# Kernel tuning notes

Hardware: AMD Instinct MI355X
Metric: run time of the kernel (lower is better)

## Reference

```python
import jax, jax.numpy as jnp
import numpy as np

NUM_TAGS = 64
HIDDEN = 768
INTERMEDIATE = 3072
TAGGING_RATE = 1.0
LN_EPS = 1e-12


def layer_norm(x, g, b):
    mu = jnp.mean(x, axis=-1, keepdims=True)
    var = jnp.mean(jnp.square(x - mu), axis=-1, keepdims=True)
    return (x - mu) * jax.lax.rsqrt(var + LN_EPS) * g + b


def setup_inputs() -> dict:
    key = jax.random.key(0)
    ks = jax.random.split(key, 16)
    B, S, H, I = 8, 4096, HIDDEN, INTERMEDIATE
    s = 0.02
    return {
        "word_embedding": jax.random.normal(ks[0], (B, S, H), jnp.float32),
        "token_tags": jax.random.randint(ks[1], (B, S), 0, NUM_TAGS, jnp.int32),
        "tag_mask": jax.random.randint(ks[2], (B, S), 0, 2, jnp.int32),
        # learned params
        "tag_emb": jax.random.normal(ks[3], (NUM_TAGS, H), jnp.float32) * s,
        "Wv": jax.random.normal(ks[4], (H, H), jnp.float32) * s,   # v_proj (applied as x @ Wv)
        "bv": jnp.zeros((H,), jnp.float32),
        "Wo": jax.random.normal(ks[5], (H, H), jnp.float32) * s,   # out_proj
        "bo": jnp.zeros((H,), jnp.float32),
        "ln1_g": jnp.ones((H,), jnp.float32),
        "ln1_b": jnp.zeros((H,), jnp.float32),
        "W1": jax.random.normal(ks[6], (H, I), jnp.float32) * s,
        "b1": jnp.zeros((I,), jnp.float32),
        "W2": jax.random.normal(ks[7], (I, H), jnp.float32) * s,
        "b2": jnp.zeros((H,), jnp.float32),
        "ln2_g": jnp.ones((H,), jnp.float32),
        "ln2_b": jnp.zeros((H,), jnp.float32),
    }


def reference(word_embedding, token_tags, tag_mask, tag_emb, Wv, bv, Wo, bo,
              ln1_g, ln1_b, W1, b1, W2, b2, ln2_g, ln2_b):
    # MHA with a single key/value: softmax over one key == 1 for every head,
    # so attention_output = out_proj(v_proj(tag_embedding[tag])), independent of q.
    per_tag = (tag_emb @ Wv + bv) @ Wo + bo              # [num_tags, H]
    taged = per_tag[token_tags] * tag_mask[..., None].astype(word_embedding.dtype)  # [B,S,H]
    x = word_embedding + taged * TAGGING_RATE            # dropout is identity in eval
    x = layer_norm(x, ln1_g, ln1_b)
    ff = jax.nn.relu(x @ W1 + b1) @ W2 + b2              # feed_forward
    out = layer_norm(ff + x, ln2_g, ln2_b)
    return out
```

## Files before the change

### kernel.cpp

```cpp
#include <hip/hip_runtime.h>
#include <hip/hip_bf16.h>
#include <cstdint>
#include <cstddef>

typedef __hip_bfloat16 bf16;
typedef __attribute__((ext_vector_type(8))) short short8;
typedef __attribute__((ext_vector_type(4))) float f32x4;

__device__ __forceinline__ void gload_lds16(const void* g, void* l) {
    __builtin_amdgcn_global_load_lds((const __attribute__((address_space(1))) void*)g,
                                     (__attribute__((address_space(3))) void*)l,
                                     16, 0, 0);
}

__device__ __forceinline__ void vm_wait6() { asm volatile("s_waitcnt vmcnt(6)" ::: "memory"); }
__device__ __forceinline__ void vm_wait0() { asm volatile("s_waitcnt vmcnt(0)" ::: "memory"); }
#define SBAR  asm volatile("s_barrier" ::: "memory")
#define LGKM0 asm volatile("s_waitcnt lgkmcnt(0)" ::: "memory")

__device__ __forceinline__ unsigned short f2bf_bits(float f) {
    bf16 h = __float2bfloat16(f);
    return *reinterpret_cast<unsigned short*>(&h);
}

__global__ __launch_bounds__(256)
void transpose_cvt(const float* __restrict__ in, bf16* __restrict__ out, int R, int C)
{
    __shared__ float tile[32][33];
    const int tx = threadIdx.x & 31;
    const int ty = threadIdx.x >> 5;
    const int c0 = blockIdx.x * 32;
    const int r0 = blockIdx.y * 32;
    #pragma unroll
    for (int j = 0; j < 32; j += 8)
        tile[ty + j][tx] = in[(size_t)(r0 + ty + j) * C + c0 + tx];
    __syncthreads();
    #pragma unroll
    for (int j = 0; j < 32; j += 8)
        out[(size_t)(c0 + ty + j) * R + r0 + tx] = __float2bfloat16(tile[tx][ty + j]);
}

__global__ __launch_bounds__(256)
void tag_gemm_a(const float* __restrict__ te, const float* __restrict__ Wv,
                const float* __restrict__ bv, float* __restrict__ t1)
{
    const int idx = blockIdx.x * 256 + threadIdx.x;
    const int i = idx / 768, j = idx - i * 768;
    float acc = bv[j];
    const float* a = te + (size_t)i * 768;
    for (int k = 0; k < 768; ++k)
        acc += a[k] * Wv[(size_t)k * 768 + j];
    t1[idx] = acc;
}

__global__ __launch_bounds__(256)
void tag_gemm_b(const float* __restrict__ t1, const float* __restrict__ Wo,
                const float* __restrict__ bo, float* __restrict__ ptab)
{
    const int idx = blockIdx.x * 256 + threadIdx.x;
    const int i = idx / 768, j = idx - i * 768;
    float acc = bo[j];
    const float* a = t1 + (size_t)i * 768;
    for (int k = 0; k < 768; ++k)
        acc += a[k] * Wo[(size_t)k * 768 + j];
    ptab[idx] = acc;
}

__global__ __launch_bounds__(192)
void addtag_ln(const float* __restrict__ we, const int* __restrict__ tags,
               const int* __restrict__ mask, const float* __restrict__ ptab,
               const float* __restrict__ g, const float* __restrict__ b,
               bf16* __restrict__ out)
{
    const int row = blockIdx.x;
    const int t = threadIdx.x;
    const int lane = t & 63, wid = t >> 6;
    const float msk = (float)mask[row];
    const float4 wv = ((const float4*)(we + (size_t)row * 768))[t];
    const float4 pv = ((const float4*)(ptab + (size_t)tags[row] * 768))[t];
    float4 x;
    x.x = wv.x + msk * pv.x;  x.y = wv.y + msk * pv.y;
    x.z = wv.z + msk * pv.z;  x.w = wv.w + msk * pv.w;
    float s  = x.x + x.y + x.z + x.w;
    float s2 = x.x * x.x + x.y * x.y + x.z * x.z + x.w * x.w;
    #pragma unroll
    for (int o = 32; o > 0; o >>= 1) { s += __shfl_down(s, o); s2 += __shfl_down(s2, o); }
    __shared__ float ls[3], ls2[3];
    if (lane == 0) { ls[wid] = s; ls2[wid] = s2; }
    __syncthreads();
    s  = ls[0] + ls[1] + ls[2];
    s2 = ls2[0] + ls2[1] + ls2[2];
    const float mean = s * (1.f / 768.f);
    float var = s2 * (1.f / 768.f) - mean * mean;
    var = var < 0.f ? 0.f : var;
    const float inv = 1.f / sqrtf(var + 1e-12f);
    const float4 gv = ((const float4*)g)[t];
    const float4 bv = ((const float4*)b)[t];
    uint2 o2;
    o2.x = (unsigned)f2bf_bits((x.x - mean) * inv * gv.x + bv.x)
         | ((unsigned)f2bf_bits((x.y - mean) * inv * gv.y + bv.y) << 16);
    o2.y = (unsigned)f2bf_bits((x.z - mean) * inv * gv.z + bv.z)
         | ((unsigned)f2bf_bits((x.w - mean) * inv * gv.w + bv.w) << 16);
    ((uint2*)(out + (size_t)row * 768))[t] = o2;
}

__global__ __launch_bounds__(192)
void ln_inplace(float* __restrict__ y, const float* __restrict__ g, const float* __restrict__ b)
{
    const int row = blockIdx.x;
    const int t = threadIdx.x;
    const int lane = t & 63, wid = t >> 6;
    float4* yr = (float4*)(y + (size_t)row * 768);
    const float4 x = yr[t];
    float s  = x.x + x.y + x.z + x.w;
    float s2 = x.x * x.x + x.y * x.y + x.z * x.z + x.w * x.w;
    #pragma unroll
    for (int o = 32; o > 0; o >>= 1) { s += __shfl_down(s, o); s2 += __shfl_down(s2, o); }
    __shared__ float ls[3], ls2[3];
    if (lane == 0) { ls[wid] = s; ls2[wid] = s2; }
    __syncthreads();
    s  = ls[0] + ls[1] + ls[2];
    s2 = ls2[0] + ls2[1] + ls2[2];
    const float mean = s * (1.f / 768.f);
    float var = s2 * (1.f / 768.f) - mean * mean;
    var = var < 0.f ? 0.f : var;
    const float inv = 1.f / sqrtf(var + 1e-12f);
    const float4 gv = ((const float4*)g)[t];
    const float4 bv = ((const float4*)b)[t];
    float4 o;
    o.x = (x.x - mean) * inv * gv.x + bv.x;
    o.y = (x.y - mean) * inv * gv.y + bv.y;
    o.z = (x.z - mean) * inv * gv.z + bv.z;
    o.w = (x.w - mean) * inv * gv.w + bv.w;
    yr[t] = o;
}

template<int EPI, typename OutT>
__global__ __launch_bounds__(512, 2)
void gemm256(const bf16* __restrict__ A, const bf16* __restrict__ Bt,
             const float* __restrict__ bias, const bf16* __restrict__ resid,
             OutT* __restrict__ C, int N, int K, int nbx)
{
    extern __shared__ char smem[];
    char* const AsB = smem;
    char* const BsB = smem + 65536;

    const int t    = threadIdx.x;
    const int lane = t & 63;
    const int wid  = t >> 6;
    const int quad = lane >> 4;
    const int lr   = lane & 15;
    const int wmRow = (wid >> 2) * 128;
    const int wnRow = (wid & 3) * 64;

    const int nwg = gridDim.x;
    const int swz = (blockIdx.x & 7) * (nwg >> 3) + (blockIdx.x >> 3);
    const int bx = swz % nbx;
    const int by = swz / nbx;
    const int rowBase = by * 256;
    const int colBase = bx * 256;

    const char* const Ab = (const char*)(A + (size_t)rowBase * K);
    const char* const Bb = (const char*)(Bt + (size_t)colBase * K);
    const int strideB = K * 2;
    const int nkt = K >> 6;

    f32x4 acc[8][4] = {};

    const int i0 = t, i1 = t + 512;
    const int r0 = i0 >> 3, r1 = i1 >> 3;
    const int sc0 = ((i0 & 7) ^ (r0 & 7)) * 16;
    const int sc1 = ((i1 & 7) ^ (r1 & 7)) * 16;

    #define STAGE_A(buf_, kt_, h_) do {                                          \
        const int kb_ = (kt_) * 128;                                             \
        gload_lds16(Ab + (size_t)((h_)*128 + r0) * strideB + kb_ + sc0,          \
                    AsB + (buf_)*32768 + (h_)*16384 + i0*16);                    \
        gload_lds16(Ab + (size_t)((h_)*128 + r1) * strideB + kb_ + sc1,          \
                    AsB + (buf_)*32768 + (h_)*16384 + i1*16);                    \
    } while (0)
    #define STAGE_B(buf_, kt_, h_) do {                                          \
        const int kb_ = (kt_) * 128;                                             \
        gload_lds16(Bb + (size_t)((h_)*128 + r0) * strideB + kb_ + sc0,          \
                    BsB + (buf_)*32768 + (h_)*16384 + i0*16);                    \
        gload_lds16(Bb + (size_t)((h_)*128 + r1) * strideB + kb_ + sc1,          \
                    BsB + (buf_)*32768 + (h_)*16384 + i1*16);                    \
    } while (0)

    short8 af0[8], af1[8], bf0[4], bf1[4];
    #define RD_A(buf_, ks_, dst_) do {                                           \
        const int cch_ = (ks_)*4 + quad;                                         \
        _Pragma("unroll")                                                        \
        for (int mi = 0; mi < 8; ++mi) {                                         \
            const int R_ = wmRow + mi*16 + lr;                                   \
            dst_[mi] = *(const short8*)(AsB + (buf_)*32768 + R_*128 +            \
                                        ((cch_ ^ (R_ & 7)) * 16));               \
        }                                                                        \
    } while (0)
    #define RD_B(buf_, ks_, dst_) do {                                           \
        const int cch_ = (ks_)*4 + quad;                                         \
        _Pragma("unroll")                                                        \
        for (int ni = 0; ni < 4; ++ni) {                                         \
            const int R_ = wnRow + ni*16 + lr;                                   \
            dst_[ni] = *(const short8*)(BsB + (buf_)*32768 + R_*128 +            \
                                        ((cch_ ^ (R_ & 7)) * 16));               \
        }                                                                        \
    } while (0)
    #define MFMA8x2(AF_, BF_, n0_) do {                                          \
        __builtin_amdgcn_s_setprio(1);                                           \
        _Pragma("unroll")                                                        \
        for (int mi = 0; mi < 8; ++mi) {                                         \
            acc[mi][(n0_)]   = __builtin_amdgcn_mfma_f32_16x16x32_bf16(          \
                AF_[mi], BF_[(n0_)],   acc[mi][(n0_)],   0, 0, 0);               \
            acc[mi][(n0_)+1] = __builtin_amdgcn_mfma_f32_16x16x32_bf16(          \
                AF_[mi], BF_[(n0_)+1], acc[mi][(n0_)+1], 0, 0, 0);               \
        }                                                                        \
        __builtin_amdgcn_s_setprio(0);                                           \
    } while (0)

    STAGE_A(0, 0, 0); STAGE_A(0, 0, 1); STAGE_B(0, 0, 0); STAGE_B(0, 0, 1);
    if (nkt > 1) { STAGE_A(1, 1, 0); STAGE_A(1, 1, 1); STAGE_B(1, 1, 0); }

    for (int kt = 0; kt < nkt; ++kt) {
        const int buf = kt & 1;
        if (kt == nkt - 1) vm_wait0(); else vm_wait6();
        SBAR;
        RD_A(buf, 0, af0);
        RD_B(buf, 0, bf0);
        if (kt + 1 < nkt) STAGE_B(buf ^ 1, kt + 1, 1);
        MFMA8x2(af0, bf0, 0);
        SBAR;
        RD_A(buf, 1, af1);
        RD_B(buf, 1, bf1);
        MFMA8x2(af0, bf0, 2);
        LGKM0;
        SBAR;
        if (kt + 2 < nkt) { STAGE_A(buf, kt + 2, 0); STAGE_A(buf, kt + 2, 1); }
        MFMA8x2(af1, bf1, 0);
        SBAR;
        if (kt + 2 < nkt) STAGE_B(buf, kt + 2, 0);
        MFMA8x2(af1, bf1, 2);
    }

    #pragma unroll
    for (int ni = 0; ni < 4; ++ni) {
        const int gc = colBase + wnRow + ni * 16 + lr;
        const float bvv = bias[gc];
        #pragma unroll
        for (int mi = 0; mi < 8; ++mi) {
            const int gr0 = rowBase + wmRow + mi * 16 + quad * 4;
            #pragma unroll
            for (int r = 0; r < 4; ++r) {
                const size_t off = (size_t)(gr0 + r) * N + gc;
                float v = acc[mi][ni][r] + bvv;
                if (EPI == 0) {
                    v = v > 0.f ? v : 0.f;
                    C[off] = (OutT)__float2bfloat16(v);
                } else {
                    v += (float)resid[off];
                    C[off] = (OutT)v;
                }
            }
        }
    }
    #undef STAGE_A
    #undef STAGE_B
    #undef RD_A
    #undef RD_B
    #undef MFMA8x2
}

extern "C" void kernel_launch(void* const* d_in, const int* in_sizes, int n_in,
                              void* d_out, int out_size, void* d_ws, size_t ws_size,
                              hipStream_t stream)
{
    const float* we      = (const float*)d_in[0];
    const int*   tags    = (const int*)d_in[1];
    const int*   mask    = (const int*)d_in[2];
    const float* tag_emb = (const float*)d_in[3];
    const float* Wv      = (const float*)d_in[4];
    const float* bv      = (const float*)d_in[5];
    const float* Wo      = (const float*)d_in[6];
    const float* bo      = (const float*)d_in[7];
    const float* ln1g    = (const float*)d_in[8];
    const float* ln1b    = (const float*)d_in[9];
    const float* W1      = (const float*)d_in[10];
    const float* b1      = (const float*)d_in[11];
    const float* W2      = (const float*)d_in[12];
    const float* b2      = (const float*)d_in[13];
    const float* ln2g    = (const float*)d_in[14];
    const float* ln2b    = (const float*)d_in[15];
    float* out = (float*)d_out;

    static bool attr_set = false;
    if (!attr_set) {
        hipFuncSetAttribute(reinterpret_cast<const void*>(&gemm256<0, bf16>),
                            hipFuncAttributeMaxDynamicSharedMemorySize, 131072);
        hipFuncSetAttribute(reinterpret_cast<const void*>(&gemm256<1, float>),
                            hipFuncAttributeMaxDynamicSharedMemorySize, 131072);
        attr_set = true;
    }

    const int M = 8 * 4096;
    char* ws = (char*)d_ws;
    const size_t oT1   = 0;
    const size_t oPtab = 196608;
    const size_t oW1t  = 393216;
    const size_t oW2t  = 5111808;
    const size_t oXn   = 9830400;
    const size_t oHh   = 60162048;
    const size_t hhFull = (size_t)M * 3072 * 2;

    const int nchunk = (ws_size >= oHh + hhFull) ? 1 : 2;
    const int MC = M / nchunk;

    float* t1   = (float*)(ws + oT1);
    float* ptab = (float*)(ws + oPtab);
    bf16*  W1t  = (bf16*)(ws + oW1t);
    bf16*  W2t  = (bf16*)(ws + oW2t);
    bf16*  xn   = (bf16*)(ws + oXn);
    bf16*  hh   = (bf16*)(ws + oHh);

    transpose_cvt<<<dim3(3072 / 32, 768 / 32), 256, 0, stream>>>(W1, W1t, 768, 3072);
    transpose_cvt<<<dim3(768 / 32, 3072 / 32), 256, 0, stream>>>(W2, W2t, 3072, 768);

    tag_gemm_a<<<192, 256, 0, stream>>>(tag_emb, Wv, bv, t1);
    tag_gemm_b<<<192, 256, 0, stream>>>(t1, Wo, bo, ptab);

    addtag_ln<<<M, 192, 0, stream>>>(we, tags, mask, ptab, ln1g, ln1b, xn);

    for (int c = 0; c < nchunk; ++c) {
        const bf16* xnC = xn + (size_t)c * MC * 768;
        const int nby = MC / 256;
        gemm256<0, bf16><<<(3072 / 256) * nby, 512, 131072, stream>>>(
            xnC, W1t, b1, nullptr, hh, 3072, 768, 3072 / 256);
        gemm256<1, float><<<(768 / 256) * nby, 512, 131072, stream>>>(
            hh, W2t, b2, xnC, out + (size_t)c * MC * 768, 768, 3072, 768 / 256);
    }

    ln_inplace<<<M, 192, 0, stream>>>(out, ln2g, ln2b);
}
```

Baseline: 748.9 us.

## Restructure GEMM main loop into quadrant-wise LDS reads with deeper prefetch waits

```diff
diff --git a/kernel.cpp b/kernel.cpp
--- a/kernel.cpp
+++ b/kernel.cpp
@@ -13,10 +13,11 @@
                                      16, 0, 0);
 }
 
-__device__ __forceinline__ void vm_wait6() { asm volatile("s_waitcnt vmcnt(6)" ::: "memory"); }
+__device__ __forceinline__ void vm_wait8() { asm volatile("s_waitcnt vmcnt(8)" ::: "memory"); }
 __device__ __forceinline__ void vm_wait0() { asm volatile("s_waitcnt vmcnt(0)" ::: "memory"); }
-#define SBAR  asm volatile("s_barrier" ::: "memory")
-#define LGKM0 asm volatile("s_waitcnt lgkmcnt(0)" ::: "memory")
+#define SBAR   asm volatile("s_barrier" ::: "memory")
+#define LGKM0  asm volatile("s_waitcnt lgkmcnt(0)" ::: "memory")
+#define SCHED0 __builtin_amdgcn_sched_barrier(0)
 
 __device__ __forceinline__ unsigned short f2bf_bits(float f) {
     bf16 h = __float2bfloat16(f);
@@ -187,59 +188,79 @@
                     BsB + (buf_)*32768 + (h_)*16384 + i1*16);                    \
     } while (0)
 
-    short8 af0[8], af1[8], bf0[4], bf1[4];
-    #define RD_A(buf_, ks_, dst_) do {                                           \
-        const int cch_ = (ks_)*4 + quad;                                         \
+    short8 afA[4][2], afB[4][2], bfA[2][2], bfB[2][2];
+    #define RD_AH(buf_, half_, dst_) do {                                        \
         _Pragma("unroll")                                                        \
-        for (int mi = 0; mi < 8; ++mi) {                                         \
-            const int R_ = wmRow + mi*16 + lr;                                   \
-            dst_[mi] = *(const short8*)(AsB + (buf_)*32768 + R_*128 +            \
-                                        ((cch_ ^ (R_ & 7)) * 16));               \
+        for (int mi = 0; mi < 4; ++mi) {                                         \
+            const int R_ = wmRow + ((half_)*4 + mi)*16 + lr;                     \
+            _Pragma("unroll")                                                    \
+            for (int ks_ = 0; ks_ < 2; ++ks_)                                    \
+                dst_[mi][ks_] = *(const short8*)(AsB + (buf_)*32768 + R_*128 +   \
+                                       (((ks_*4 + quad) ^ (R_ & 7)) * 16));      \
         }                                                                        \
     } while (0)
-    #define RD_B(buf_, ks_, dst_) do {                                           \
-        const int cch_ = (ks_)*4 + quad;                                         \
+    #define RD_BH(buf_, half_, dst_) do {                                        \
         _Pragma("unroll")                                                        \
-        for (int ni = 0; ni < 4; ++ni) {                                         \
-            const int R_ = wnRow + ni*16 + lr;                                   \
-            dst_[ni] = *(const short8*)(BsB + (buf_)*32768 + R_*128 +            \
-                                        ((cch_ ^ (R_ & 7)) * 16));               \
+        for (int ni = 0; ni < 2; ++ni) {                                         \
+            const int R_ = wnRow + ((half_)*2 + ni)*16 + lr;                     \
+            _Pragma("unroll")                                                    \
+            for (int ks_ = 0; ks_ < 2; ++ks_)                                    \
+                dst_[ni][ks_] = *(const short8*)(BsB + (buf_)*32768 + R_*128 +   \
+                                       (((ks_*4 + quad) ^ (R_ & 7)) * 16));      \
         }                                                                        \
     } while (0)
-    #define MFMA8x2(AF_, BF_, n0_) do {                                          \
+    #define MFMA_Q(AF_, BF_, MB_, NB_) do {                                      \
         __builtin_amdgcn_s_setprio(1);                                           \
         _Pragma("unroll")                                                        \
-        for (int mi = 0; mi < 8; ++mi) {                                         \
-            acc[mi][(n0_)]   = __builtin_amdgcn_mfma_f32_16x16x32_bf16(          \
-                AF_[mi], BF_[(n0_)],   acc[mi][(n0_)],   0, 0, 0);               \
-            acc[mi][(n0_)+1] = __builtin_amdgcn_mfma_f32_16x16x32_bf16(          \
-                AF_[mi], BF_[(n0_)+1], acc[mi][(n0_)+1], 0, 0, 0);               \
+        for (int mi = 0; mi < 4; ++mi) {                                         \
+            _Pragma("unroll")                                                    \
+            for (int ni = 0; ni < 2; ++ni) {                                     \
+                acc[(MB_)+mi][(NB_)+ni] = __builtin_amdgcn_mfma_f32_16x16x32_bf16( \
+                    AF_[mi][0], BF_[ni][0], acc[(MB_)+mi][(NB_)+ni], 0, 0, 0);   \
+                acc[(MB_)+mi][(NB_)+ni] = __builtin_amdgcn_mfma_f32_16x16x32_bf16( \
+                    AF_[mi][1], BF_[ni][1], acc[(MB_)+mi][(NB_)+ni], 0, 0, 0);   \
+            }                                                                    \
         }                                                                        \
         __builtin_amdgcn_s_setprio(0);                                           \
     } while (0)
 
     STAGE_A(0, 0, 0); STAGE_A(0, 0, 1); STAGE_B(0, 0, 0); STAGE_B(0, 0, 1);
-    if (nkt > 1) { STAGE_A(1, 1, 0); STAGE_A(1, 1, 1); STAGE_B(1, 1, 0); }
+    if (nkt > 1) {
+        STAGE_B(1, 1, 0); STAGE_B(1, 1, 1); STAGE_A(1, 1, 0); STAGE_A(1, 1, 1);
+        vm_wait8();
+    } else {
+        vm_wait0();
+    }
+    SCHED0;
+    SBAR;
 
     for (int kt = 0; kt < nkt; ++kt) {
         const int buf = kt & 1;
-        if (kt == nkt - 1) vm_wait0(); else vm_wait6();
-        SBAR;
-        RD_A(buf, 0, af0);
-        RD_B(buf, 0, bf0);
-        if (kt + 1 < nkt) STAGE_B(buf ^ 1, kt + 1, 1);
-        MFMA8x2(af0, bf0, 0);
-        SBAR;
-        RD_A(buf, 1, af1);
-        RD_B(buf, 1, bf1);
-        MFMA8x2(af0, bf0, 2);
-        LGKM0;
+        RD_AH(buf, 0, afA);
+        RD_BH(buf, 0, bfA);
+        SBAR;
+        LGKM0; SCHED0;
+        MFMA_Q(afA, bfA, 0, 0);
+        SBAR;
+        RD_BH(buf, 1, bfB);
+        SBAR;
+        LGKM0; SCHED0;
+        MFMA_Q(afA, bfB, 0, 2);
+        SBAR;
+        RD_AH(buf, 1, afB);
+        if (kt + 2 < nkt) { STAGE_B(buf, kt + 2, 0); STAGE_B(buf, kt + 2, 1); }
+        SBAR;
+        LGKM0; SCHED0;
+        MFMA_Q(afB, bfB, 4, 2);
         SBAR;
         if (kt + 2 < nkt) { STAGE_A(buf, kt + 2, 0); STAGE_A(buf, kt + 2, 1); }
-        MFMA8x2(af1, bf1, 0);
-        SBAR;
-        if (kt + 2 < nkt) STAGE_B(buf, kt + 2, 0);
-        MFMA8x2(af1, bf1, 2);
+        SBAR;
+        MFMA_Q(afB, bfA, 4, 0);
+        if (kt + 1 < nkt) {
+            if (kt + 2 < nkt) vm_wait8(); else vm_wait0();
+            SCHED0;
+        }
+        SBAR;
     }
 
     #pragma unroll
@@ -265,9 +286,9 @@
     }
     #undef STAGE_A
     #undef STAGE_B
-    #undef RD_A
-    #undef RD_B
-    #undef MFMA8x2
+    #undef RD_AH
+    #undef RD_BH
+    #undef MFMA_Q
 }
 
 extern "C" void kernel_launch(void* const* d_in, const int* in_sizes, int n_in,
```

Result: slower. 829.1 us (+10.7%).
